# Kernel tuning notes

Hardware: AMD Instinct MI355X
Metric: run time of the kernel (lower is better)

Reference implementation:

```python
import jax, jax.numpy as jnp
import numpy as np

B, N, NS, H, HD, G = 2, 4096, 32, 8, 32, 16


def setup_inputs() -> dict:
    key = jax.random.key(0)
    ks = jax.random.split(key, 8)
    q = jax.random.normal(ks[0], (B, N, H, HD), dtype=jnp.float32)
    k_neigh = jax.random.normal(ks[1], (B, N, NS, H * HD), dtype=jnp.float32)
    v_neigh = jax.random.normal(ks[2], (B, N, NS, H * HD), dtype=jnp.float32)
    geo_f = jax.random.normal(ks[3], (B, N, NS, G), dtype=jnp.float32)
    # att_conv_fea: Linear(NS, NS) -> Linear(NS, 1), applied over the neighbor axis
    W1 = jax.random.normal(ks[4], (NS, NS), dtype=jnp.float32) * (NS ** -0.5)
    b1 = jax.random.normal(ks[5], (NS,), dtype=jnp.float32) * 0.02
    W2 = jax.random.normal(ks[6], (NS,), dtype=jnp.float32) * (NS ** -0.5)
    b2 = jnp.zeros((), dtype=jnp.float32)
    return {"q": q, "k_neigh": k_neigh, "v_neigh": v_neigh, "geo_f": geo_f,
            "W1": W1, "b1": b1, "W2": W2, "b2": b2}


def reference(q, k_neigh, v_neigh, geo_f, W1, b1, W2, b2):
    b, n, h, hd = q.shape
    ns = k_neigh.shape[2]
    g = geo_f.shape[-1]
    scale = hd ** -0.5
    k = k_neigh.reshape(b, n, ns, h, hd)
    v = v_neigh.reshape(b, n, ns, h, hd)
    # subtract kernel: [B, N, NS, H, HD]
    w = (q * scale)[:, :, None, :, :] - k
    geo = jnp.broadcast_to(geo_f[:, :, :, None, :], (b, n, ns, h, g))
    we = jnp.concatenate([w, geo], axis=-1)          # [B, N, NS, H, D]
    # MLP over the neighbor (NS) axis, per (b, n, head, feature) slice:
    # h1[b,n,t,h,d] = sum_s we[b,n,s,h,d] * W1[t,s] + b1[t]
    h1 = jnp.einsum('bnshd,ts->bnthd', we, W1) + b1[None, None, :, None, None]
    score = jnp.einsum('bnthd,t->bnhd', h1, W2) + b2  # [B, N, H, D]
    we = we * score[:, :, None, :, :]                 # broadcast over NS
    weight = jnp.sum(we, axis=-1)                     # [B, N, NS, H]
    attn = jax.nn.softmax(weight, axis=2)             # softmax over neighbors
    out = jnp.einsum('bnsh,bnshd->bnhd', attn, v)     # [B, N, H, HD]
    return out
```

## Files before the change

kernel.cpp:

```cpp
#include <hip/hip_runtime.h>

constexpr int NSC = 32;
constexpr int CC  = 256;
constexpr int HDD = 32;
constexpr int HH  = 8;
constexpr int GG  = 16;
constexpr int GEO_PAD = 17;

__global__ __launch_bounds__(256, 4)
void geoneigh_att_kernel(const float* __restrict__ q,
                         const float* __restrict__ kng,
                         const float* __restrict__ vng,
                         const float* __restrict__ geo,
                         const float* __restrict__ W1,
                         const float* __restrict__ b1,
                         const float* __restrict__ W2,
                         const float* __restrict__ b2,
                         float* __restrict__ out)
{
    __shared__ float lds_k[NSC * CC];
    __shared__ float lds_score[CC];
    __shared__ float lds_geo[NSC * GEO_PAD];
    __shared__ float lds_w[NSC * HH];
    __shared__ float lds_attn[NSC * HH];
    __shared__ float lds_weff[NSC];
    __shared__ float lds_sgeo[GG];
    __shared__ float lds_beff[1];

    const int t  = threadIdx.x;
    const int bn = blockIdx.x;
    const size_t tokKV = (size_t)bn * (NSC * CC);
    const float* kp = kng + tokKV;
    const float* vp = vng + tokKV;
    const float* qp = q   + (size_t)bn * CC;
    const float* gp = geo + (size_t)bn * (NSC * GG);

    const float4* kp4 = (const float4*)kp;
    float4* lk4 = (float4*)lds_k;
#pragma unroll
    for (int i = 0; i < 8; ++i) lk4[t + 256 * i] = kp4[t + 256 * i];

    const int sgrp = t >> 6, c4 = t & 63;
    const float4* vp4 = (const float4*)vp;
    float4 vreg[8];
#pragma unroll
    for (int kk = 0; kk < 8; ++kk) vreg[kk] = vp4[(sgrp + 4 * kk) * 64 + c4];

    const float qv = qp[t] * 0.17677669529663687f;

    if (t < 128) {
        float4 gg = ((const float4*)gp)[t];
        int s = t >> 2, off = (t & 3) * 4;
        float* dst = &lds_geo[s * GEO_PAD + off];
        dst[0] = gg.x; dst[1] = gg.y; dst[2] = gg.z; dst[3] = gg.w;
    }
    if (t < 32) {
        float acc = 0.f;
#pragma unroll
        for (int tt = 0; tt < 32; ++tt) acc += W2[tt] * W1[tt * 32 + t];
        lds_weff[t] = acc;
    } else if (t == 32) {
        float acc = b2[0];
#pragma unroll
        for (int tt = 0; tt < 32; ++tt) acc += W2[tt] * b1[tt];
        lds_beff[0] = acc;
    }
    __syncthreads();

    const float beff = lds_beff[0];
    float kd = 0.f, wsum = 0.f;
#pragma unroll
    for (int s = 0; s < NSC; ++s) {
        float w = lds_weff[s];
        wsum += w;
        kd += lds_k[s * CC + t] * w;
    }
    lds_score[t] = qv * wsum - kd + beff;

    if (t < GG) {
        float sg = beff;
#pragma unroll
        for (int s = 0; s < NSC; ++s) sg += lds_geo[s * GEO_PAD + t] * lds_weff[s];
        lds_sgeo[t] = sg;
    }
    __syncthreads();

    {
        const int s = t >> 3, h = t & 7;
        const int kbase = s * CC + h * HDD;
        const int sbase = h * HDD;
        float kw = 0.f;
#pragma unroll
        for (int i = 0; i < HDD; ++i) {
            int d = (i + t) & 31;
            kw += lds_k[kbase + d] * lds_score[sbase + d];
        }
        float gws = 0.f;
#pragma unroll
        for (int g = 0; g < GG; ++g) gws += lds_geo[s * GEO_PAD + g] * lds_sgeo[g];
        lds_w[t] = gws - kw;
    }
    __syncthreads();

    if (t < HH) {
        float m = -1e30f;
#pragma unroll
        for (int s = 0; s < NSC; ++s) m = fmaxf(m, lds_w[s * HH + t]);
        float e[NSC];
        float sum = 0.f;
#pragma unroll
        for (int s = 0; s < NSC; ++s) { e[s] = expf(lds_w[s * HH + t] - m); sum += e[s]; }
        float r = 1.f / sum;
#pragma unroll
        for (int s = 0; s < NSC; ++s) lds_attn[s * HH + t] = e[s] * r;
    }
    __syncthreads();

    const int h2 = c4 >> 3;
    float4 acc = make_float4(0.f, 0.f, 0.f, 0.f);
#pragma unroll
    for (int kk = 0; kk < 8; ++kk) {
        float a = lds_attn[(sgrp + 4 * kk) * HH + h2];
        acc.x += a * vreg[kk].x;
        acc.y += a * vreg[kk].y;
        acc.z += a * vreg[kk].z;
        acc.w += a * vreg[kk].w;
    }
    float4* part4 = (float4*)lds_k;
    part4[sgrp * 64 + c4] = acc;
    __syncthreads();
    if (t < 64) {
        float4 r0 = part4[t], r1 = part4[64 + t], r2 = part4[128 + t], r3 = part4[192 + t];
        float4 o = make_float4(r0.x + r1.x + r2.x + r3.x,
                               r0.y + r1.y + r2.y + r3.y,
                               r0.z + r1.z + r2.z + r3.z,
                               r0.w + r1.w + r2.w + r3.w);
        ((float4*)(out + (size_t)bn * CC))[t] = o;
    }
}

extern "C" void kernel_launch(void* const* d_in, const int* in_sizes, int n_in,
                              void* d_out, int out_size, void* d_ws, size_t ws_size,
                              hipStream_t stream) {
    const float* q   = (const float*)d_in[0];
    const float* kng = (const float*)d_in[1];
    const float* vng = (const float*)d_in[2];
    const float* geo = (const float*)d_in[3];
    const float* W1  = (const float*)d_in[4];
    const float* b1  = (const float*)d_in[5];
    const float* W2  = (const float*)d_in[6];
    const float* b2  = (const float*)d_in[7];
    float* out = (float*)d_out;

    const int tokens = 2 * 4096;
    geoneigh_att_kernel<<<tokens, 256, 0, stream>>>(q, kng, vng, geo, W1, b1, W2, b2, out);
}
```

Before: 533.3 us.

## Replace LDS staging with per-head register/shuffle pipeline and precomputed weights

The kernel drops all shared memory and barriers. Each thread keeps one channel's 32 neighbor keys in registers, and each 32-lane group, which equals one head, does the per-neighbor reductions, softmax and geo terms with cross-lane shuffles. The effective MLP weights are computed once by a tiny setup kernel into workspace instead of in every block, and V is read directly with scalar loads in the final weighted sum. The aim is to remove LDS traffic, barriers and serial single-thread softmax work, at the cost of many shuffle reductions, scalar (non-vectorized) global loads, and an extra launch.

```diff
diff --git a/kernel.cpp b/kernel.cpp
--- a/kernel.cpp
+++ b/kernel.cpp
@@ -2,141 +2,99 @@
 
 constexpr int NSC = 32;
 constexpr int CC  = 256;
-constexpr int HDD = 32;
-constexpr int HH  = 8;
 constexpr int GG  = 16;
-constexpr int GEO_PAD = 17;
+
+
+__global__ void setup_weff(const float* __restrict__ W1, const float* __restrict__ b1,
+                           const float* __restrict__ W2, const float* __restrict__ b2,
+                           float* __restrict__ ws) {
+    const int t = threadIdx.x;
+    if (t < 32) {
+        float acc = 0.f;
+#pragma unroll
+        for (int tt = 0; tt < 32; ++tt) acc += W2[tt] * W1[tt * 32 + t];
+        ws[t] = acc;
+        float wsum = acc;
+#pragma unroll
+        for (int m = 16; m >= 1; m >>= 1) wsum += __shfl_xor(wsum, m, 32);
+        if (t == 0) {
+            float beff = b2[0];
+#pragma unroll
+            for (int tt = 0; tt < 32; ++tt) beff += W2[tt] * b1[tt];
+            ws[32] = beff;
+            ws[33] = wsum;
+        }
+    }
+}
 
 __global__ __launch_bounds__(256, 4)
 void geoneigh_att_kernel(const float* __restrict__ q,
                          const float* __restrict__ kng,
                          const float* __restrict__ vng,
                          const float* __restrict__ geo,
-                         const float* __restrict__ W1,
-                         const float* __restrict__ b1,
-                         const float* __restrict__ W2,
-                         const float* __restrict__ b2,
+                         const float* __restrict__ ws,
                          float* __restrict__ out)
 {
-    __shared__ float lds_k[NSC * CC];
-    __shared__ float lds_score[CC];
-    __shared__ float lds_geo[NSC * GEO_PAD];
-    __shared__ float lds_w[NSC * HH];
-    __shared__ float lds_attn[NSC * HH];
-    __shared__ float lds_weff[NSC];
-    __shared__ float lds_sgeo[GG];
-    __shared__ float lds_beff[1];
-
     const int t  = threadIdx.x;
     const int bn = blockIdx.x;
-    const size_t tokKV = (size_t)bn * (NSC * CC);
-    const float* kp = kng + tokKV;
-    const float* vp = vng + tokKV;
-    const float* qp = q   + (size_t)bn * CC;
+    const int c  = t;
+    const int sl = t & 31;
+
+    const size_t kvbase = (size_t)bn * (NSC * CC);
+    const float* kp = kng + kvbase;
+    const float* vp = vng + kvbase;
     const float* gp = geo + (size_t)bn * (NSC * GG);
 
-    const float4* kp4 = (const float4*)kp;
-    float4* lk4 = (float4*)lds_k;
+    float kreg[NSC];
 #pragma unroll
-    for (int i = 0; i < 8; ++i) lk4[t + 256 * i] = kp4[t + 256 * i];
+    for (int s = 0; s < NSC; ++s) kreg[s] = kp[s * CC + c];
 
-    const int sgrp = t >> 6, c4 = t & 63;
-    const float4* vp4 = (const float4*)vp;
-    float4 vreg[8];
+    float georeg[GG];
 #pragma unroll
-    for (int kk = 0; kk < 8; ++kk) vreg[kk] = vp4[(sgrp + 4 * kk) * 64 + c4];
+    for (int g = 0; g < GG; ++g) georeg[g] = gp[sl * GG + g];
 
-    const float qv = qp[t] * 0.17677669529663687f;
+    const float weffr = ws[sl];
+    const float beff  = ws[32];
+    const float wsum  = ws[33];
+    const float qv = q[(size_t)bn * CC + c] * 0.17677669529663687f;
 
-    if (t < 128) {
-        float4 gg = ((const float4*)gp)[t];
-        int s = t >> 2, off = (t & 3) * 4;
-        float* dst = &lds_geo[s * GEO_PAD + off];
-        dst[0] = gg.x; dst[1] = gg.y; dst[2] = gg.z; dst[3] = gg.w;
+    float kd = 0.f;
+#pragma unroll
+    for (int s = 0; s < NSC; ++s) kd += kreg[s] * ws[s];
+    const float score = qv * wsum - kd + beff;
+
+    float gw = 0.f;
+#pragma unroll
+    for (int g = 0; g < GG; ++g) {
+        float p = georeg[g] * weffr;
+#pragma unroll
+        for (int m = 16; m >= 1; m >>= 1) p += __shfl_xor(p, m, 32);
+        gw += georeg[g] * (p + beff);
     }
-    if (t < 32) {
-        float acc = 0.f;
-#pragma unroll
-        for (int tt = 0; tt < 32; ++tt) acc += W2[tt] * W1[tt * 32 + t];
-        lds_weff[t] = acc;
-    } else if (t == 32) {
-        float acc = b2[0];
-#pragma unroll
-        for (int tt = 0; tt < 32; ++tt) acc += W2[tt] * b1[tt];
-        lds_beff[0] = acc;
-    }
-    __syncthreads();
 
-    const float beff = lds_beff[0];
-    float kd = 0.f, wsum = 0.f;
+    float wsel = 0.f;
 #pragma unroll
     for (int s = 0; s < NSC; ++s) {
-        float w = lds_weff[s];
-        wsum += w;
-        kd += lds_k[s * CC + t] * w;
+        float p = kreg[s] * score;
+#pragma unroll
+        for (int m = 16; m >= 1; m >>= 1) p += __shfl_xor(p, m, 32);
+        const float w_s = __shfl(gw, s, 32) - p;
+        wsel = (sl == s) ? w_s : wsel;
     }
-    lds_score[t] = qv * wsum - kd + beff;
 
-    if (t < GG) {
-        float sg = beff;
+    float mx = wsel;
 #pragma unroll
-        for (int s = 0; s < NSC; ++s) sg += lds_geo[s * GEO_PAD + t] * lds_weff[s];
-        lds_sgeo[t] = sg;
-    }
-    __syncthreads();
+    for (int m = 16; m >= 1; m >>= 1) mx = fmaxf(mx, __shfl_xor(mx, m, 32));
+    const float e = __expf(wsel - mx);
+    float se = e;
+#pragma unroll
+    for (int m = 16; m >= 1; m >>= 1) se += __shfl_xor(se, m, 32);
+    const float attn = e / se;
 
-    {
-        const int s = t >> 3, h = t & 7;
-        const int kbase = s * CC + h * HDD;
-        const int sbase = h * HDD;
-        float kw = 0.f;
+    float acc = 0.f;
 #pragma unroll
-        for (int i = 0; i < HDD; ++i) {
-            int d = (i + t) & 31;
-            kw += lds_k[kbase + d] * lds_score[sbase + d];
-        }
-        float gws = 0.f;
-#pragma unroll
-        for (int g = 0; g < GG; ++g) gws += lds_geo[s * GEO_PAD + g] * lds_sgeo[g];
-        lds_w[t] = gws - kw;
-    }
-    __syncthreads();
-
-    if (t < HH) {
-        float m = -1e30f;
-#pragma unroll
-        for (int s = 0; s < NSC; ++s) m = fmaxf(m, lds_w[s * HH + t]);
-        float e[NSC];
-        float sum = 0.f;
-#pragma unroll
-        for (int s = 0; s < NSC; ++s) { e[s] = expf(lds_w[s * HH + t] - m); sum += e[s]; }
-        float r = 1.f / sum;
-#pragma unroll
-        for (int s = 0; s < NSC; ++s) lds_attn[s * HH + t] = e[s] * r;
-    }
-    __syncthreads();
-
-    const int h2 = c4 >> 3;
-    float4 acc = make_float4(0.f, 0.f, 0.f, 0.f);
-#pragma unroll
-    for (int kk = 0; kk < 8; ++kk) {
-        float a = lds_attn[(sgrp + 4 * kk) * HH + h2];
-        acc.x += a * vreg[kk].x;
-        acc.y += a * vreg[kk].y;
-        acc.z += a * vreg[kk].z;
-        acc.w += a * vreg[kk].w;
-    }
-    float4* part4 = (float4*)lds_k;
-    part4[sgrp * 64 + c4] = acc;
-    __syncthreads();
-    if (t < 64) {
-        float4 r0 = part4[t], r1 = part4[64 + t], r2 = part4[128 + t], r3 = part4[192 + t];
-        float4 o = make_float4(r0.x + r1.x + r2.x + r3.x,
-                               r0.y + r1.y + r2.y + r3.y,
-                               r0.z + r1.z + r2.z + r3.z,
-                               r0.w + r1.w + r2.w + r3.w);
-        ((float4*)(out + (size_t)bn * CC))[t] = o;
-    }
+    for (int s = 0; s < NSC; ++s) acc += __shfl(attn, s, 32) * vp[s * CC + c];
+    out[(size_t)bn * CC + c] = acc;
 }
 
 extern "C" void kernel_launch(void* const* d_in, const int* in_sizes, int n_in,
@@ -151,7 +109,9 @@
     const float* W2  = (const float*)d_in[6];
     const float* b2  = (const float*)d_in[7];
     float* out = (float*)d_out;
+    float* ws  = (float*)d_ws;
 
+    setup_weff<<<1, 64, 0, stream>>>(W1, b1, W2, b2, ws);
     const int tokens = 2 * 4096;
-    geoneigh_att_kernel<<<tokens, 256, 0, stream>>>(q, kng, vng, geo, W1, b1, W2, b2, out);
+    geoneigh_att_kernel<<<tokens, 256, 0, stream>>>(q, kng, vng, geo, ws, out);
 }
```

New measurement: 545.0 us. 2.2% more time.
